# Kernel optimization log

Hardware: AMD Instinct MI355X
Metric: run time of the kernel (lower is better)

The kernel has to match this reference:

```python
import jax, jax.numpy as jnp
import numpy as np

NUM_EXPERTS = 64
TOP_K = 2
AUX_LOSS_COEF = 0.01
HIDDEN = 2048
BATCH, SEQ = 4, 4096


def setup_inputs() -> dict:
    key = jax.random.key(0)
    k1, k2 = jax.random.split(key)
    hidden_states = jax.random.normal(k1, (BATCH, SEQ, HIDDEN), dtype=jnp.float32)
    # nn.Linear(hidden, num_experts, bias=False) weight: [E, H]
    gate_w = jax.random.normal(k2, (NUM_EXPERTS, HIDDEN), dtype=jnp.float32) / np.sqrt(HIDDEN)
    return {"hidden_states": hidden_states, "gate_w": gate_w}


def reference(hidden_states, gate_w):
    B, S, H = hidden_states.shape
    E, K = NUM_EXPERTS, TOP_K
    # gate: [B,S,H] x [E,H]^T -> [B,S,E]
    router_logits = jnp.einsum('bsh,eh->bse', hidden_states, gate_w)
    router_probs = jax.nn.softmax(router_logits, axis=-1)
    top_k_probs, expert_indices = jax.lax.top_k(router_probs, K)  # [B,S,K]
    top_k_probs = top_k_probs / jnp.sum(top_k_probs, axis=-1, keepdims=True)
    # aux load-balancing loss
    expert_mask = jax.nn.one_hot(expert_indices, E, dtype=router_probs.dtype).sum(axis=-2)  # [B,S,E]
    tokens_per_expert = expert_mask.sum(axis=(0, 1))          # [E]
    prob_per_expert = router_probs.mean(axis=(0, 1))          # [E]
    num_tokens = B * S
    aux_loss = E * jnp.sum(tokens_per_expert * prob_per_expert) / num_tokens
    router_loss = aux_loss * AUX_LOSS_COEF
    return top_k_probs, expert_indices, router_loss
```

## Files before the change

### kernel.cpp

```cpp
#include <hip/hip_runtime.h>
#include <math.h>

#define TOKENS 16384
#define HID    2048
#define NCH    32
#define TPB    64

typedef float f4 __attribute__((ext_vector_type(4)));
typedef short s8v __attribute__((ext_vector_type(8)));

#define WS_W1    0
#define WS_W2    262144
#define WS_BP    524288
#define WS_G2    786432

__device__ __forceinline__ unsigned short bf16rne(float x) {
  unsigned u = __float_as_uint(x);
  return (unsigned short)((u + 0x7FFFu + ((u >> 16) & 1u)) >> 16);
}

__device__ __forceinline__ void gl16(const void* g, const void* l) {
  __builtin_amdgcn_global_load_lds(
      (const __attribute__((address_space(1))) void*)g,
      (__attribute__((address_space(3))) void*)l, 16, 0, 0);
}

#define BARK(N) { asm volatile("s_waitcnt vmcnt(" #N ") lgkmcnt(0)" ::: "memory"); \
  __builtin_amdgcn_sched_barrier(0); __builtin_amdgcn_s_barrier(); \
  __builtin_amdgcn_sched_barrier(0); }

__global__ __launch_bounds__(256) void k_pack(const float* __restrict__ gw,
                                              unsigned short* __restrict__ w1,
                                              unsigned short* __restrict__ w2) {
  int gid = blockIdx.x * 256 + threadIdx.x;
  int m = gid * 8;
  f4 a = *(const f4*)(gw + m);
  f4 b = *(const f4*)(gw + m + 4);
  float av[8] = {a.x, a.y, a.z, a.w, b.x, b.y, b.z, b.w};
  unsigned short p1[8], p2[8];
  #pragma unroll
  for (int i = 0; i < 8; ++i) {
    unsigned short h = bf16rne(av[i]);
    p1[i] = h;
    float r = av[i] - __uint_as_float((unsigned)h << 16);
    p2[i] = bf16rne(r);
  }
  *(s8v*)(w1 + m) = *(s8v*)p1;
  *(s8v*)(w2 + m) = *(s8v*)p2;
}

__global__ __launch_bounds__(512, 1) void k_main(const float* __restrict__ hid,
                                                 const unsigned short* __restrict__ w1,
                                                 const unsigned short* __restrict__ w2,
                                                 float* __restrict__ out,
                                                 float* __restrict__ bp) {
  __shared__ __align__(16) char lds[131072];
  const int tid = threadIdx.x, wave = tid >> 6, lane = tid & 63;
  const int th = wave >> 1, eh = wave & 1;
  const int l15 = lane & 15, ks = lane >> 4;
  const int tok0 = blockIdx.x * TPB;

  const char* hb = (const char*)hid;
  size_t asrc[2]; int adst[2];
  #pragma unroll
  for (int j = 0; j < 2; ++j) {
    int u = j * 512 + tid;
    int row = u >> 4, g = u & 15;
    asrc[j] = (size_t)(tok0 + row) * 8192 + (size_t)((g ^ (row & 3)) << 4);
    adst[j] = u * 16;
  }
  const char* w1b = (const char*)w1;
  const char* w2b = (const char*)w2;
  const int eB = tid >> 3, gB = tid & 7;
  const size_t bsrc = (size_t)eB * 4096 + (size_t)((gB ^ (eB & 3)) << 4);

  f4 acc[2] = {{0.f,0.f,0.f,0.f},{0.f,0.f,0.f,0.f}};
  const int arow = th * 16 + l15, asw = arow & 3;
  const int be[2] = {eh * 32 + l15, eh * 32 + 16 + l15};

  auto stage = [&](int c, int bufb) {
    #pragma unroll
    for (int j = 0; j < 2; ++j)
      gl16(hb + asrc[j] + (size_t)c * 256, lds + bufb + adst[j]);
    gl16(w1b + bsrc + (size_t)c * 128, lds + bufb + 16384 + tid * 16);
    gl16(w2b + bsrc + (size_t)c * 128, lds + bufb + 24576 + tid * 16);
  };

  auto compute = [&](int bufb) {
    #pragma unroll
    for (int s = 0; s < 2; ++s) {
      int g0 = (s * 8 + ks * 2) ^ asw;
      int g1 = (s * 8 + ks * 2 + 1) ^ asw;
      f4 a0 = *(const f4*)(lds + bufb + arow * 256 + g0 * 16);
      f4 a1 = *(const f4*)(lds + bufb + arow * 256 + g1 * 16);
      float av[8] = {a0.x, a0.y, a0.z, a0.w, a1.x, a1.y, a1.z, a1.w};
      unsigned short p1[8], p2[8];
      #pragma unroll
      for (int i = 0; i < 8; ++i) {
        unsigned short h = bf16rne(av[i]);
        p1[i] = h;
        float r = av[i] - __uint_as_float((unsigned)h << 16);
        p2[i] = bf16rne(r);
      }
      s8v af1 = *(s8v*)p1;
      s8v af2 = *(s8v*)p2;
      #pragma unroll
      for (int nj = 0; nj < 2; ++nj) {
        int g = (s * 4 + ks) ^ (be[nj] & 3);
        s8v bw1 = *(const s8v*)(lds + bufb + 16384 + be[nj] * 128 + g * 16);
        s8v bw2 = *(const s8v*)(lds + bufb + 24576 + be[nj] * 128 + g * 16);
        acc[nj] = __builtin_amdgcn_mfma_f32_16x16x32_bf16(af1, bw1, acc[nj], 0, 0, 0);
        acc[nj] = __builtin_amdgcn_mfma_f32_16x16x32_bf16(af1, bw2, acc[nj], 0, 0, 0);
        acc[nj] = __builtin_amdgcn_mfma_f32_16x16x32_bf16(af2, bw1, acc[nj], 0, 0, 0);
      }
    }
  };

  stage(0, 0);
  stage(1, 32768);
  stage(2, 65536);
  BARK(8);

  for (int c = 0; c < NCH; ++c) {
    const int bufb = (c & 3) * 32768;
    if (c + 3 < NCH) stage(c + 3, ((c + 3) & 3) * 32768);
    compute(bufb);
    if (c + 3 < NCH)      { BARK(8); }
    else if (c + 2 < NCH) { BARK(4); }
    else                  { BARK(0); }
  }

  float* lf = (float*)lds;
  #pragma unroll
  for (int nj = 0; nj < 2; ++nj)
    #pragma unroll
    for (int r = 0; r < 4; ++r)
      lf[(th * 16 + ks * 4 + r) * 68 + eh * 32 + nj * 16 + l15] = acc[nj][r];
  __syncthreads();

  float spacc = 0.f, cntacc = 0.f;
  for (int it = 0; it < 8; ++it) {
    const int tl = wave * 8 + it;
    float lg = lf[tl * 68 + lane];
    float m1 = lg;
    #pragma unroll
    for (int d = 1; d < 64; d <<= 1) m1 = fmaxf(m1, __shfl_xor(m1, d));
    int c0 = (lg == m1) ? lane : 64;
    #pragma unroll
    for (int d = 1; d < 64; d <<= 1) c0 = min(c0, __shfl_xor(c0, d));
    float lx1 = (lane == c0) ? -INFINITY : lg;
    float m2 = lx1;
    #pragma unroll
    for (int d = 1; d < 64; d <<= 1) m2 = fmaxf(m2, __shfl_xor(m2, d));
    int c1 = (lx1 == m2) ? lane : 64;
    #pragma unroll
    for (int d = 1; d < 64; d <<= 1) c1 = min(c1, __shfl_xor(c1, d));

    float p = __expf(lg - m1);
    float Z = p;
    #pragma unroll
    for (int d = 1; d < 64; d <<= 1) Z += __shfl_xor(Z, d);
    spacc = fmaf(p, 1.f / Z, spacc);
    cntacc += ((lane == c0) ? 1.f : 0.f) + ((lane == c1) ? 1.f : 0.f);

    float gr = __expf(m2 - m1);
    float r0 = 1.f / (1.f + gr);
    if (lane == 0) {
      int t = tok0 + tl;
      out[(size_t)t * 2]     = r0;
      out[(size_t)t * 2 + 1] = gr * r0;
      out[(size_t)TOKENS * 2 + t * 2]     = (float)c0;
      out[(size_t)TOKENS * 2 + t * 2 + 1] = (float)c1;
    }
  }

  float* red = lf + 4352;
  red[wave * 128 + lane]      = spacc;
  red[wave * 128 + 64 + lane] = cntacc;
  __syncthreads();
  if (tid < 128) {
    float s = 0.f;
    #pragma unroll
    for (int w = 0; w < 8; ++w) s += red[w * 128 + tid];
    bp[(size_t)blockIdx.x * 128 + tid] = s;
  }
}

__global__ __launch_bounds__(128) void k_loss1(const float* __restrict__ bp,
                                               float* __restrict__ g2) {
  float s = 0.f;
  #pragma unroll 4
  for (int j = 0; j < 8; ++j)
    s += bp[(size_t)(blockIdx.x * 8 + j) * 128 + threadIdx.x];
  g2[(size_t)blockIdx.x * 128 + threadIdx.x] = s;
}

__global__ __launch_bounds__(128) void k_loss2(const float* __restrict__ g2,
                                               float* __restrict__ out) {
  const int tid = threadIdx.x;
  float s = 0.f;
  #pragma unroll 8
  for (int j = 0; j < 32; ++j) s += g2[(size_t)j * 128 + tid];
  __shared__ float red[128];
  red[tid] = s;
  __syncthreads();
  if (tid < 64) {
    float v = red[tid] * red[64 + tid];
    #pragma unroll
    for (int d = 1; d < 64; d <<= 1) v += __shfl_xor(v, d);
    if (tid == 0)
      out[(size_t)TOKENS * 4] = 0.01f * 64.f * v / (16384.f * 16384.f);
  }
}

extern "C" void kernel_launch(void* const* d_in, const int* in_sizes, int n_in,
                              void* d_out, int out_size, void* d_ws, size_t ws_size,
                              hipStream_t stream) {
  (void)in_sizes; (void)n_in; (void)out_size; (void)ws_size;
  const float* hid = (const float*)d_in[0];
  const float* gw  = (const float*)d_in[1];
  float* out = (float*)d_out;
  char* ws = (char*)d_ws;
  unsigned short* w1 = (unsigned short*)(ws + WS_W1);
  unsigned short* w2 = (unsigned short*)(ws + WS_W2);
  float* bp    = (float*)(ws + WS_BP);
  float* g2    = (float*)(ws + WS_G2);

  k_pack <<<64, 256, 0, stream>>>(gw, w1, w2);
  k_main <<<256, 512, 0, stream>>>(hid, w1, w2, out, bp);
  k_loss1<<<32, 128, 0, stream>>>(bp, g2);
  k_loss2<<<1, 128, 0, stream>>>(g2, out);
}
```

Before: 54.23 us.

## Double tokens per block and switch to three-stage pipeline

Measured after the change: 72.37 us. 1.33x slower.

```diff
diff --git a/kernel.cpp b/kernel.cpp
--- a/kernel.cpp
+++ b/kernel.cpp
@@ -4,7 +4,7 @@
 #define TOKENS 16384
 #define HID    2048
 #define NCH    32
-#define TPB    64
+#define TPB    128
 
 typedef float f4 __attribute__((ext_vector_type(4)));
 typedef short s8v __attribute__((ext_vector_type(8)));
@@ -54,16 +54,15 @@
                                                  const unsigned short* __restrict__ w2,
                                                  float* __restrict__ out,
                                                  float* __restrict__ bp) {
-  __shared__ __align__(16) char lds[131072];
+  __shared__ __align__(16) char lds[147456];
   const int tid = threadIdx.x, wave = tid >> 6, lane = tid & 63;
-  const int th = wave >> 1, eh = wave & 1;
   const int l15 = lane & 15, ks = lane >> 4;
   const int tok0 = blockIdx.x * TPB;
 
   const char* hb = (const char*)hid;
-  size_t asrc[2]; int adst[2];
+  size_t asrc[4]; int adst[4];
   #pragma unroll
-  for (int j = 0; j < 2; ++j) {
+  for (int j = 0; j < 4; ++j) {
     int u = j * 512 + tid;
     int row = u >> 4, g = u & 15;
     asrc[j] = (size_t)(tok0 + row) * 8192 + (size_t)((g ^ (row & 3)) << 4);
@@ -74,16 +73,15 @@
   const int eB = tid >> 3, gB = tid & 7;
   const size_t bsrc = (size_t)eB * 4096 + (size_t)((gB ^ (eB & 3)) << 4);
 
-  f4 acc[2] = {{0.f,0.f,0.f,0.f},{0.f,0.f,0.f,0.f}};
-  const int arow = th * 16 + l15, asw = arow & 3;
-  const int be[2] = {eh * 32 + l15, eh * 32 + 16 + l15};
+  f4 acc[4] = {{0.f,0.f,0.f,0.f},{0.f,0.f,0.f,0.f},{0.f,0.f,0.f,0.f},{0.f,0.f,0.f,0.f}};
+  const int arow = wave * 16 + l15, asw = arow & 3;
 
   auto stage = [&](int c, int bufb) {
     #pragma unroll
-    for (int j = 0; j < 2; ++j)
+    for (int j = 0; j < 4; ++j)
       gl16(hb + asrc[j] + (size_t)c * 256, lds + bufb + adst[j]);
-    gl16(w1b + bsrc + (size_t)c * 128, lds + bufb + 16384 + tid * 16);
-    gl16(w2b + bsrc + (size_t)c * 128, lds + bufb + 24576 + tid * 16);
+    gl16(w1b + bsrc + (size_t)c * 128, lds + bufb + 32768 + tid * 16);
+    gl16(w2b + bsrc + (size_t)c * 128, lds + bufb + 40960 + tid * 16);
   };
 
   auto compute = [&](int bufb) {
@@ -105,10 +103,11 @@
       s8v af1 = *(s8v*)p1;
       s8v af2 = *(s8v*)p2;
       #pragma unroll
-      for (int nj = 0; nj < 2; ++nj) {
-        int g = (s * 4 + ks) ^ (be[nj] & 3);
-        s8v bw1 = *(const s8v*)(lds + bufb + 16384 + be[nj] * 128 + g * 16);
-        s8v bw2 = *(const s8v*)(lds + bufb + 24576 + be[nj] * 128 + g * 16);
+      for (int nj = 0; nj < 4; ++nj) {
+        int e = nj * 16 + l15;
+        int g = (s * 4 + ks) ^ (e & 3);
+        s8v bw1 = *(const s8v*)(lds + bufb + 32768 + e * 128 + g * 16);
+        s8v bw2 = *(const s8v*)(lds + bufb + 40960 + e * 128 + g * 16);
         acc[nj] = __builtin_amdgcn_mfma_f32_16x16x32_bf16(af1, bw1, acc[nj], 0, 0, 0);
         acc[nj] = __builtin_amdgcn_mfma_f32_16x16x32_bf16(af1, bw2, acc[nj], 0, 0, 0);
         acc[nj] = __builtin_amdgcn_mfma_f32_16x16x32_bf16(af2, bw1, acc[nj], 0, 0, 0);
@@ -117,30 +116,35 @@
   };
 
   stage(0, 0);
-  stage(1, 32768);
-  stage(2, 65536);
-  BARK(8);
+  stage(1, 49152);
+  BARK(6);
 
   for (int c = 0; c < NCH; ++c) {
-    const int bufb = (c & 3) * 32768;
-    if (c + 3 < NCH) stage(c + 3, ((c + 3) & 3) * 32768);
-    compute(bufb);
-    if (c + 3 < NCH)      { BARK(8); }
-    else if (c + 2 < NCH) { BARK(4); }
-    else                  { BARK(0); }
-  }
-
+    const int bufb = (c % 3) * 49152;
+    if (c + 2 < NCH) {
+      stage(c + 2, ((c + 2) % 3) * 49152);
+      compute(bufb);
+      BARK(6);
+    } else if (c + 1 < NCH) {
+      compute(bufb);
+      BARK(0);
+    } else {
+      compute(bufb);
+    }
+  }
+
+  __syncthreads();
   float* lf = (float*)lds;
   #pragma unroll
-  for (int nj = 0; nj < 2; ++nj)
+  for (int nj = 0; nj < 4; ++nj)
     #pragma unroll
     for (int r = 0; r < 4; ++r)
-      lf[(th * 16 + ks * 4 + r) * 68 + eh * 32 + nj * 16 + l15] = acc[nj][r];
+      lf[(wave * 16 + ks * 4 + r) * 68 + nj * 16 + l15] = acc[nj][r];
   __syncthreads();
 
   float spacc = 0.f, cntacc = 0.f;
-  for (int it = 0; it < 8; ++it) {
-    const int tl = wave * 8 + it;
+  for (int it = 0; it < 16; ++it) {
+    const int tl = wave * 16 + it;
     float lg = lf[tl * 68 + lane];
     float m1 = lg;
     #pragma unroll
@@ -174,7 +178,7 @@
     }
   }
 
-  float* red = lf + 4352;
+  float* red = lf + 8704;
   red[wave * 128 + lane]      = spacc;
   red[wave * 128 + 64 + lane] = cntacc;
   __syncthreads();
@@ -200,7 +204,7 @@
   const int tid = threadIdx.x;
   float s = 0.f;
   #pragma unroll 8
-  for (int j = 0; j < 32; ++j) s += g2[(size_t)j * 128 + tid];
+  for (int j = 0; j < 16; ++j) s += g2[(size_t)j * 128 + tid];
   __shared__ float red[128];
   red[tid] = s;
   __syncthreads();
@@ -227,7 +231,7 @@
   float* g2    = (float*)(ws + WS_G2);
 
   k_pack <<<64, 256, 0, stream>>>(gw, w1, w2);
-  k_main <<<256, 512, 0, stream>>>(hid, w1, w2, out, bp);
-  k_loss1<<<32, 128, 0, stream>>>(bp, g2);
+  k_main <<<128, 512, 0, stream>>>(hid, w1, w2, out, bp);
+  k_loss1<<<16, 128, 0, stream>>>(bp, g2);
   k_loss2<<<1, 128, 0, stream>>>(g2, out);
 }
```
